# Optimization experiments

Hardware: AMD Instinct MI355X
Metric: run time of the kernel (lower is better)

## Reference

```python
import jax, jax.numpy as jnp
import numpy as np

N = 50000          # nodes
E = 800000         # edges per meta-path (avg degree 16)
M = 2              # meta-paths
IN = 256           # in_size
H, D = 4, 64       # heads, out_size per head
HD = H * D
SEM_HID = 128      # SemanticAttention hidden_size
NEG_SLOPE = 0.2    # DGL GATConv default LeakyReLU slope


def setup_inputs() -> dict:
    key = jax.random.key(0)
    ks = jax.random.split(key, 10)
    h = jax.random.normal(ks[0], (N, IN), dtype=jnp.float32)
    src = jax.random.randint(ks[1], (M, E), 0, N, dtype=jnp.int32)
    dst = jax.random.randint(ks[2], (M, E), 0, N, dtype=jnp.int32)
    # per-meta-path GATConv params
    W = jax.random.normal(ks[3], (M, IN, HD), dtype=jnp.float32) * (1.0 / np.sqrt(IN))
    attn_l = jax.random.normal(ks[4], (M, H, D), dtype=jnp.float32) * 0.1
    attn_r = jax.random.normal(ks[5], (M, H, D), dtype=jnp.float32) * 0.1
    # semantic attention params
    sem_w1 = jax.random.normal(ks[6], (HD, SEM_HID), dtype=jnp.float32) * (1.0 / np.sqrt(HD))
    sem_b1 = jnp.zeros((SEM_HID,), dtype=jnp.float32)
    sem_w2 = jax.random.normal(ks[7], (SEM_HID, 1), dtype=jnp.float32) * (1.0 / np.sqrt(SEM_HID))
    return {"h": h, "src": src, "dst": dst, "W": W, "attn_l": attn_l,
            "attn_r": attn_r, "sem_w1": sem_w1, "sem_b1": sem_b1, "sem_w2": sem_w2}


def _gat_conv(h, s, d, W_i, al, ar):
    # h: [N, IN]; s, d: [E] int edge endpoints; returns [N, H*D]
    feat = (h @ W_i).reshape(N, H, D)                       # [N,H,D]
    el = jnp.einsum('nhd,hd->nh', feat, al)                 # [N,H]
    er = jnp.einsum('nhd,hd->nh', feat, ar)                 # [N,H]
    e = jax.nn.leaky_relu(el[s] + er[d], NEG_SLOPE)         # [E,H]
    # edge softmax over incoming edges of each dst node
    m = jax.ops.segment_max(e, d, num_segments=N)           # [N,H]
    m = jax.lax.stop_gradient(jnp.where(jnp.isfinite(m), m, 0.0))
    ex = jnp.exp(e - m[d])                                  # [E,H]
    den = jax.ops.segment_sum(ex, d, num_segments=N)        # [N,H]
    alpha = ex / jnp.maximum(den[d], 1e-9)                  # [E,H]
    msg = alpha[:, :, None] * feat[s]                       # [E,H,D]
    rst = jax.ops.segment_sum(msg, d, num_segments=N)       # [N,H,D] (zero for 0-in-degree)
    return jax.nn.elu(rst).reshape(N, HD)


def reference(h, src, dst, W, attn_l, attn_r, sem_w1, sem_b1, sem_w2):
    embs = [_gat_conv(h, src[i], dst[i], W[i], attn_l[i], attn_r[i]) for i in range(M)]
    z = jnp.stack(embs, axis=1)                             # [N,M,HD]
    # semantic attention: w = mean over nodes of MLP score per meta-path
    w = jnp.einsum('nms,so->mo', jnp.tanh(jnp.einsum('nmd,ds->nms', z, sem_w1) + sem_b1), sem_w2) / N  # [M,1]
    beta = jax.nn.softmax(w, axis=0)                        # [M,1]
    return jnp.einsum('nmd,mo->nd', z, beta)                # [N,HD]
```

## Files before the change

kernel.cpp:

```cpp
#include <hip/hip_runtime.h>
#include <hip/hip_bf16.h>

#define NND 50000
#define NE 800000
#define NM 2
#define INF 256
#define NH 4
#define HDIM 256
#define SHID 128
#define SLOPE 0.2f
#define NB 196
#define NREP 8

typedef unsigned short u16;
typedef __attribute__((ext_vector_type(8))) short bf16x8;
typedef __attribute__((ext_vector_type(4))) float f32x4;

__device__ __forceinline__ float us2f(u16 u) {
  union { unsigned int i; float f; } v; v.i = ((unsigned int)u) << 16; return v.f;
}
__device__ __forceinline__ u16 f2us(float f) {
  union { float f; unsigned int i; } v; v.f = f;
  unsigned int r = v.i + 0x7FFFu + ((v.i >> 16) & 1u);
  return (u16)(r >> 16);
}

#define GLDS(g, l) __builtin_amdgcn_global_load_lds( \
    (const __attribute__((address_space(1))) unsigned int*)(g), \
    (__attribute__((address_space(3))) unsigned int*)(l), 16, 0, 0)

__global__ __launch_bounds__(256) void kh_cvt(const float* __restrict__ h,
                                              u16* __restrict__ hb) {
  const size_t i = ((size_t)blockIdx.x * 256 + threadIdx.x) * 8;
  float4 a = *(const float4*)(h + i);
  float4 b = *(const float4*)(h + i + 4);
  bf16x8 r;
  r[0] = f2us(a.x); r[1] = f2us(a.y); r[2] = f2us(a.z); r[3] = f2us(a.w);
  r[4] = f2us(b.x); r[5] = f2us(b.y); r[6] = f2us(b.z); r[7] = f2us(b.w);
  *(bf16x8*)(hb + i) = r;
}

__global__ __launch_bounds__(256) void kt_w(const float* __restrict__ W,
                                            u16* __restrict__ Wt) {
  __shared__ u16 tile[64][65];
  const int t = threadIdx.x;
  const int k0 = blockIdx.x * 64, n0 = blockIdx.y * 64;
  const float* Wm = W + (size_t)blockIdx.z * 65536;
  u16* Wtm = Wt + (size_t)blockIdx.z * 65536;
  const int lr = t >> 2, c0 = (t & 3) * 16;
#pragma unroll
  for (int i = 0; i < 16; ++i)
    tile[lr][c0 + i] = f2us(Wm[(size_t)(k0 + lr) * 256 + n0 + c0 + i]);
  __syncthreads();
#pragma unroll
  for (int i = 0; i < 16; ++i)
    Wtm[(size_t)(n0 + lr) * 256 + k0 + c0 + i] = tile[c0 + i][lr];
}

__global__ __launch_bounds__(256) void kt_w1(const float* __restrict__ w1,
                                             u16* __restrict__ w1t) {
  __shared__ u16 tile[64][65];
  const int t = threadIdx.x;
  const int k0 = blockIdx.x * 64, j0 = blockIdx.y * 64;
  const int lr = t >> 2, c0 = (t & 3) * 16;
#pragma unroll
  for (int i = 0; i < 16; ++i)
    tile[lr][c0 + i] = f2us(w1[(size_t)(k0 + lr) * SHID + j0 + c0 + i]);
  __syncthreads();
#pragma unroll
  for (int i = 0; i < 16; ++i)
    w1t[(size_t)(j0 + lr) * 256 + k0 + c0 + i] = tile[c0 + i][lr];
}

__global__ __launch_bounds__(256) void kc_hist_both(const int* __restrict__ dst_all,
                                                    int* __restrict__ hrep) {
  int e = blockIdx.x * 256 + threadIdx.x;
  int p = (e >= NE) ? 1 : 0;
  int rep = blockIdx.x & (NREP - 1);
  atomicAdd(hrep + ((size_t)p * NREP + rep) * (NND + 1) + dst_all[e] + 1, 1);
}

__global__ __launch_bounds__(256) void ks1(const int* __restrict__ hrep,
                                           int* __restrict__ rowptr,
                                           int* __restrict__ bsum) {
  __shared__ int wsums[4];
  const int t = threadIdx.x;
  const int p = blockIdx.x / NB, lb = blockIdx.x % NB;
  int* rp = rowptr + (size_t)p * (NND + 1);
  const int i = lb * 256 + t + 1;
  int v = 0;
  if (i <= NND) {
    const int* hp = hrep + (size_t)p * NREP * (NND + 1);
#pragma unroll
    for (int r = 0; r < NREP; ++r) v += hp[(size_t)r * (NND + 1) + i];
  }
  const int lane = t & 63, wid = t >> 6;
#pragma unroll
  for (int o = 1; o < 64; o <<= 1) {
    int u = __shfl_up(v, o, 64);
    if (lane >= o) v += u;
  }
  if (lane == 63) wsums[wid] = v;
  __syncthreads();
  if (t == 0) {
    int s = 0;
#pragma unroll
    for (int w = 0; w < 4; ++w) { int x = wsums[w]; wsums[w] = s; s += x; }
    bsum[blockIdx.x] = s;
  }
  __syncthreads();
  v += wsums[wid];
  if (i <= NND) rp[i] = v;
}

__global__ __launch_bounds__(256) void ks3(int* __restrict__ rowptr,
                                           const int* __restrict__ bsum,
                                           int* __restrict__ cursor) {
  __shared__ int redp[4];
  __shared__ int off_s;
  const int t = threadIdx.x;
  const int p = blockIdx.x / NB, lb = blockIdx.x % NB;
  int* rp = rowptr + (size_t)p * (NND + 1);
  int* cp = cursor + (size_t)p * NND;
  int partial = (t < lb) ? bsum[p * NB + t] : 0;
  const int lane = t & 63, wid = t >> 6;
#pragma unroll
  for (int o = 32; o; o >>= 1) partial += __shfl_xor(partial, o, 64);
  if (lane == 0) redp[wid] = partial;
  __syncthreads();
  if (t == 0) off_s = redp[0] + redp[1] + redp[2] + redp[3];
  __syncthreads();
  const int off = off_s;
  const int i = lb * 256 + t + 1;
  if (i <= NND) {
    int v = rp[i] + off;
    rp[i] = v;
    if (i < NND) cp[i] = v;
    if (i == 1) { cp[0] = 0; rp[0] = 0; }
  }
}

__global__ __launch_bounds__(256) void kc_scatter(
    const int* __restrict__ src, const int* __restrict__ dst,
    int* __restrict__ cursor, int* __restrict__ col,
    const float* __restrict__ el, const float* __restrict__ er,
    float* __restrict__ exps)
{
  int e = blockIdx.x * 256 + threadIdx.x;
  if (e >= NE) return;
  int s = src[e], d = dst[e];
  int pos = atomicAdd(cursor + d, 1);
  col[pos] = s;
  float4 a = *(const float4*)(el + s * 4);
  float4 b = *(const float4*)(er + d * 4);
  float4 r;
  float x;
  x = a.x + b.x; x = x > 0.f ? x : SLOPE * x; r.x = __expf(x);
  x = a.y + b.y; x = x > 0.f ? x : SLOPE * x; r.y = __expf(x);
  x = a.z + b.z; x = x > 0.f ? x : SLOPE * x; r.z = __expf(x);
  x = a.w + b.w; x = x > 0.f ? x : SLOPE * x; r.w = __expf(x);
  *(float4*)(exps + (size_t)pos * 4) = r;
}

__global__ __launch_bounds__(256) void k1_mfma(
    const u16* __restrict__ hb, const u16* __restrict__ Wt,
    u16* __restrict__ feat)
{
  __shared__ u16 As[128 * 32];
  __shared__ u16 Bs[128 * 32];
  const int t = threadIdx.x;
  const int lane = t & 63;
  const int w = t >> 6;
  const int wr = w >> 1, wc = w & 1;
  const int row0 = blockIdx.x * 128;
  const int col0 = blockIdx.y * 128;

  const int sr = t >> 2;
  const int skb = (t & 3) * 8;

  int ra0 = row0 + sr;       if (ra0 >= NND) ra0 = NND - 1;
  int ra1 = row0 + 64 + sr;  if (ra1 >= NND) ra1 = NND - 1;
  const int cb0 = col0 + sr, cb1 = col0 + 64 + sr;

  f32x4 acc[4][4];
#pragma unroll
  for (int i = 0; i < 4; ++i)
#pragma unroll
    for (int j = 0; j < 4; ++j) acc[i][j] = (f32x4){0.f, 0.f, 0.f, 0.f};

  for (int ks = 0; ks < 8; ++ks) {
    const int kb = ks * 32 + skb;
    __syncthreads();
    GLDS(hb + (size_t)ra0 * INF + kb, As + w * 512);
    GLDS(hb + (size_t)ra1 * INF + kb, As + 2048 + w * 512);
    GLDS(Wt + (size_t)cb0 * 256 + kb, Bs + w * 512);
    GLDS(Wt + (size_t)cb1 * 256 + kb, Bs + 2048 + w * 512);
    __syncthreads();
    bf16x8 af[4], bfr[4];
#pragma unroll
    for (int mi = 0; mi < 4; ++mi)
      af[mi] = *(const bf16x8*)(As + (wr * 64 + mi * 16 + (lane & 15)) * 32 + (lane >> 4) * 8);
#pragma unroll
    for (int ni = 0; ni < 4; ++ni)
      bfr[ni] = *(const bf16x8*)(Bs + (wc * 64 + ni * 16 + (lane & 15)) * 32 + (lane >> 4) * 8);
#pragma unroll
    for (int mi = 0; mi < 4; ++mi)
#pragma unroll
      for (int ni = 0; ni < 4; ++ni)
        acc[mi][ni] = __builtin_amdgcn_mfma_f32_16x16x32_bf16(af[mi], bfr[ni], acc[mi][ni], 0, 0, 0);
  }
#pragma unroll
  for (int mi = 0; mi < 4; ++mi) {
    const int r_base = row0 + wr * 64 + mi * 16 + (lane >> 4) * 4;
#pragma unroll
    for (int i = 0; i < 4; ++i) {
      const int r = r_base + i;
      if (r < NND) {
#pragma unroll
        for (int ni = 0; ni < 4; ++ni) {
          const int c = col0 + wc * 64 + ni * 16 + (lane & 15);
          feat[(size_t)r * HDIM + c] = f2us(acc[mi][ni][i]);
        }
      }
    }
  }
}

__global__ __launch_bounds__(256) void k1b_elr(
    const u16* __restrict__ feat,
    const float* __restrict__ al, const float* __restrict__ ar,
    float* __restrict__ el, float* __restrict__ er)
{
  const int n = blockIdx.x * 4 + (threadIdx.x >> 6);
  const int lane = threadIdx.x & 63;
  ushort4 f4 = *(const ushort4*)(feat + (size_t)n * HDIM + lane * 4);
  float4 a4 = *(const float4*)(al + lane * 4);
  float4 r4 = *(const float4*)(ar + lane * 4);
  float fl = us2f(f4.x) * a4.x + us2f(f4.y) * a4.y
           + us2f(f4.z) * a4.z + us2f(f4.w) * a4.w;
  float fr = us2f(f4.x) * r4.x + us2f(f4.y) * r4.y
           + us2f(f4.z) * r4.z + us2f(f4.w) * r4.w;
#pragma unroll
  for (int o = 1; o < 16; o <<= 1) {
    fl += __shfl_xor(fl, o, 64);
    fr += __shfl_xor(fr, o, 64);
  }
  if ((lane & 15) == 0) {
    el[n * 4 + (lane >> 4)] = fl;
    er[n * 4 + (lane >> 4)] = fr;
  }
}

template<int OBF>
__global__ __launch_bounds__(256) void k3_gather(
    const int* __restrict__ rowptr, const int* __restrict__ col,
    const float* __restrict__ exps,
    const u16* __restrict__ feat, void* __restrict__ z)
{
  const int d = blockIdx.x * 4 + (threadIdx.x >> 6);
  if (d >= NND) return;
  const int lane = threadIdx.x & 63;
  const int h = lane >> 4;
  const int sub = lane & 15;
  const int beg = rowptr[d], end = rowptr[d + 1];

  float den = 0.f;
  for (int j = beg + sub; j < end; j += 16)
    den += exps[(size_t)j * 4 + h];
#pragma unroll
  for (int o = 1; o < 16; o <<= 1) den += __shfl_xor(den, o, 64);
  const float inv = 1.f / fmaxf(den, 1e-9f);

  float a0 = 0.f, a1 = 0.f, a2 = 0.f, a3 = 0.f;
  int j = beg;
  for (; j + 3 < end; j += 4) {
    int s0 = col[j], s1 = col[j + 1], s2 = col[j + 2], s3 = col[j + 3];
    float p0 = exps[(size_t)j * 4 + h] * inv;
    float p1 = exps[(size_t)(j + 1) * 4 + h] * inv;
    float p2 = exps[(size_t)(j + 2) * 4 + h] * inv;
    float p3 = exps[(size_t)(j + 3) * 4 + h] * inv;
    const ushort4 f0 = *(const ushort4*)(feat + (size_t)s0 * HDIM + lane * 4);
    const ushort4 f1 = *(const ushort4*)(feat + (size_t)s1 * HDIM + lane * 4);
    const ushort4 f2 = *(const ushort4*)(feat + (size_t)s2 * HDIM + lane * 4);
    const ushort4 f3 = *(const ushort4*)(feat + (size_t)s3 * HDIM + lane * 4);
    a0 = fmaf(p0, us2f(f0.x), a0); a1 = fmaf(p0, us2f(f0.y), a1);
    a2 = fmaf(p0, us2f(f0.z), a2); a3 = fmaf(p0, us2f(f0.w), a3);
    a0 = fmaf(p1, us2f(f1.x), a0); a1 = fmaf(p1, us2f(f1.y), a1);
    a2 = fmaf(p1, us2f(f1.z), a2); a3 = fmaf(p1, us2f(f1.w), a3);
    a0 = fmaf(p2, us2f(f2.x), a0); a1 = fmaf(p2, us2f(f2.y), a1);
    a2 = fmaf(p2, us2f(f2.z), a2); a3 = fmaf(p2, us2f(f2.w), a3);
    a0 = fmaf(p3, us2f(f3.x), a0); a1 = fmaf(p3, us2f(f3.y), a1);
    a2 = fmaf(p3, us2f(f3.z), a2); a3 = fmaf(p3, us2f(f3.w), a3);
  }
  for (; j < end; ++j) {
    int s = col[j];
    float p = exps[(size_t)j * 4 + h] * inv;
    const ushort4 f4 = *(const ushort4*)(feat + (size_t)s * HDIM + lane * 4);
    a0 = fmaf(p, us2f(f4.x), a0); a1 = fmaf(p, us2f(f4.y), a1);
    a2 = fmaf(p, us2f(f4.z), a2); a3 = fmaf(p, us2f(f4.w), a3);
  }
  a0 = a0 > 0.f ? a0 : expf(a0) - 1.f;
  a1 = a1 > 0.f ? a1 : expf(a1) - 1.f;
  a2 = a2 > 0.f ? a2 : expf(a2) - 1.f;
  a3 = a3 > 0.f ? a3 : expf(a3) - 1.f;
  const size_t idx = (size_t)d * HDIM + lane * 4;
  if (OBF) {
    ushort4 r; r.x = f2us(a0); r.y = f2us(a1); r.z = f2us(a2); r.w = f2us(a3);
    *(ushort4*)((u16*)z + idx) = r;
  } else {
    float4 r; r.x = a0; r.y = a1; r.z = a2; r.w = a3;
    *(float4*)((float*)z + idx) = r;
  }
}

template<int ZBF>
__global__ __launch_bounds__(256) void k4_mfma(
    const void* __restrict__ zsrc, const u16* __restrict__ w1t,
    const float* __restrict__ b1, const float* __restrict__ w2,
    float* __restrict__ wsum, int midx)
{
  __shared__ u16 As[128 * 32];
  __shared__ u16 Bs[128 * 32];
  __shared__ float red[4];
  const int t = threadIdx.x;
  const int lane = t & 63;
  const int w = t >> 6;
  const int wr = w >> 1, wc = w & 1;
  const int row0 = blockIdx.x * 128;
  const int sr = t >> 2;
  const int skb = (t & 3) * 8;
  int ra0 = row0 + sr;       if (ra0 >= NND) ra0 = NND - 1;
  int ra1 = row0 + 64 + sr;  if (ra1 >= NND) ra1 = NND - 1;
  const int cb0 = sr, cb1 = 64 + sr;

  f32x4 acc[4][4];
#pragma unroll
  for (int i = 0; i < 4; ++i)
#pragma unroll
    for (int j = 0; j < 4; ++j) acc[i][j] = (f32x4){0.f, 0.f, 0.f, 0.f};

  for (int ks = 0; ks < 8; ++ks) {
    const int kb = ks * 32 + skb;
    __syncthreads();
    if (ZBF) {
      GLDS((const u16*)zsrc + (size_t)ra0 * HDIM + kb, As + w * 512);
      GLDS((const u16*)zsrc + (size_t)ra1 * HDIM + kb, As + 2048 + w * 512);
    } else {
      const float* zf = (const float*)zsrc;
      float4 a = *(const float4*)(zf + (size_t)ra0 * HDIM + kb);
      float4 b = *(const float4*)(zf + (size_t)ra0 * HDIM + kb + 4);
      bf16x8 r;
      r[0] = f2us(a.x); r[1] = f2us(a.y); r[2] = f2us(a.z); r[3] = f2us(a.w);
      r[4] = f2us(b.x); r[5] = f2us(b.y); r[6] = f2us(b.z); r[7] = f2us(b.w);
      *(bf16x8*)(As + sr * 32 + skb) = r;
      a = *(const float4*)(zf + (size_t)ra1 * HDIM + kb);
      b = *(const float4*)(zf + (size_t)ra1 * HDIM + kb + 4);
      r[0] = f2us(a.x); r[1] = f2us(a.y); r[2] = f2us(a.z); r[3] = f2us(a.w);
      r[4] = f2us(b.x); r[5] = f2us(b.y); r[6] = f2us(b.z); r[7] = f2us(b.w);
      *(bf16x8*)(As + (64 + sr) * 32 + skb) = r;
    }
    GLDS(w1t + (size_t)cb0 * 256 + kb, Bs + w * 512);
    GLDS(w1t + (size_t)cb1 * 256 + kb, Bs + 2048 + w * 512);
    __syncthreads();
    bf16x8 af[4], bfr[4];
#pragma unroll
    for (int mi = 0; mi < 4; ++mi)
      af[mi] = *(const bf16x8*)(As + (wr * 64 + mi * 16 + (lane & 15)) * 32 + (lane >> 4) * 8);
#pragma unroll
    for (int ni = 0; ni < 4; ++ni)
      bfr[ni] = *(const bf16x8*)(Bs + (wc * 64 + ni * 16 + (lane & 15)) * 32 + (lane >> 4) * 8);
#pragma unroll
    for (int mi = 0; mi < 4; ++mi)
#pragma unroll
      for (int ni = 0; ni < 4; ++ni)
        acc[mi][ni] = __builtin_amdgcn_mfma_f32_16x16x32_bf16(af[mi], bfr[ni], acc[mi][ni], 0, 0, 0);
  }
  float sum = 0.f;
#pragma unroll
  for (int ni = 0; ni < 4; ++ni) {
    const int c = wc * 64 + ni * 16 + (lane & 15);
    const float b1c = b1[c], w2c = w2[c];
#pragma unroll
    for (int mi = 0; mi < 4; ++mi) {
      const int r_base = row0 + wr * 64 + mi * 16 + (lane >> 4) * 4;
#pragma unroll
      for (int i = 0; i < 4; ++i) {
        if (r_base + i < NND)
          sum += tanhf(acc[mi][ni][i] + b1c) * w2c;
      }
    }
  }
#pragma unroll
  for (int o = 32; o; o >>= 1) sum += __shfl_xor(sum, o, 64);
  if (lane == 0) red[w] = sum;
  __syncthreads();
  if (t == 0) unsafeAtomicAdd(wsum + midx, red[0] + red[1] + red[2] + red[3]);
}

__global__ __launch_bounds__(256) void k5_out(
    float* __restrict__ out, const u16* __restrict__ z1,
    const float* __restrict__ wsum)
{
  const int i = blockIdx.x * 256 + threadIdx.x;
  float w0 = wsum[0] * (1.0f / NND);
  float w1v = wsum[1] * (1.0f / NND);
  float mx = fmaxf(w0, w1v);
  float e0 = expf(w0 - mx), e1 = expf(w1v - mx);
  float inv = 1.f / (e0 + e1);
  float b0 = e0 * inv, b1 = e1 * inv;
  float4 a = ((const float4*)out)[i];
  ushort4 zb = ((const ushort4*)z1)[i];
  float4 r;
  r.x = b0 * a.x + b1 * us2f(zb.x);
  r.y = b0 * a.y + b1 * us2f(zb.y);
  r.z = b0 * a.z + b1 * us2f(zb.z);
  r.w = b0 * a.w + b1 * us2f(zb.w);
  ((float4*)out)[i] = r;
}

extern "C" void kernel_launch(void* const* d_in, const int* in_sizes, int n_in,
                              void* d_out, int out_size, void* d_ws, size_t ws_size,
                              hipStream_t stream)
{
  const float* h  = (const float*)d_in[0];
  const int* src  = (const int*)d_in[1];
  const int* dst  = (const int*)d_in[2];
  const float* W  = (const float*)d_in[3];
  const float* al = (const float*)d_in[4];
  const float* ar = (const float*)d_in[5];
  const float* w1 = (const float*)d_in[6];
  const float* b1 = (const float*)d_in[7];
  const float* w2 = (const float*)d_in[8];

  char* wsb = (char*)d_ws;
  u16*   feat   = (u16*)(wsb);
  u16*   hz     = (u16*)(wsb + 25600000);
  float* exps   = (float*)(wsb + 51200000);
  int*   col    = (int*)(wsb + 64000000);
  u16*   Wt     = (u16*)(wsb + 67200000);
  u16*   w1t    = (u16*)(wsb + 67462144);
  float* el     = (float*)(wsb + 67527680);
  float* er     = (float*)(wsb + 68327680);
  int*   rowptr = (int*)(wsb + 69127680);
  int*   cursor = (int*)(wsb + 69527688);
  float* wsum   = (float*)(wsb + 69927688);
  int*   bsum   = (int*)(wsb + 69927696);
  int*   hrep   = (int*)(wsb + 69929264);
  const size_t NEED = 73129328;
  if (ws_size < NEED) {
    hipMemsetAsync(d_out, 0x7F, (size_t)out_size * 4, stream);
    return;
  }
  u16* z1 = hz;
  float* outp = (float*)d_out;

  kh_cvt<<<6250, 256, 0, stream>>>(h, hz);
  kt_w<<<dim3(4, 4, 2), 256, 0, stream>>>(W, Wt);
  kt_w1<<<dim3(4, 2), 256, 0, stream>>>(w1, w1t);
  hipMemsetAsync(wsum, 0, 2 * sizeof(float), stream);
  hipMemsetAsync(hrep, 0, (size_t)2 * NREP * (NND + 1) * sizeof(int), stream);
  kc_hist_both<<<2 * NE / 256, 256, 0, stream>>>(dst, hrep);
  ks1<<<2 * NB, 256, 0, stream>>>(hrep, rowptr, bsum);
  ks3<<<2 * NB, 256, 0, stream>>>(rowptr, bsum, cursor);

  for (int m = 0; m < NM; ++m) {
    const int* src_m = src + (size_t)m * NE;
    const int* dst_m = dst + (size_t)m * NE;
    int* rowptr_m = rowptr + (size_t)m * (NND + 1);
    int* cursor_m = cursor + (size_t)m * NND;
    k1_mfma<<<dim3(391, 2), 256, 0, stream>>>(hz, Wt + (size_t)m * 65536, feat);
    k1b_elr<<<12500, 256, 0, stream>>>(feat, al + (size_t)m * HDIM, ar + (size_t)m * HDIM, el, er);
    kc_scatter<<<NE / 256, 256, 0, stream>>>(src_m, dst_m, cursor_m, col, el, er, exps);
    if (m == 0) {
      k3_gather<0><<<12500, 256, 0, stream>>>(rowptr_m, col, exps, feat, d_out);
      k4_mfma<0><<<391, 256, 0, stream>>>(d_out, w1t, b1, w2, wsum, 0);
    } else {
      k3_gather<1><<<12500, 256, 0, stream>>>(rowptr_m, col, exps, feat, z1);
      k4_mfma<1><<<391, 256, 0, stream>>>(z1, w1t, b1, w2, wsum, 1);
    }
  }
  k5_out<<<(NND * HDIM / 4) / 256, 256, 0, stream>>>(outp, z1, wsum);
}
```

Before: 418.5 us.

## Merge prep kernels, split scatter cursors per replica, widen GEMM K-tiles with swizzle

Three setup kernels (input cast, W transpose, w1 transpose) are merged into one launch. The scatter step now uses NREP per-replica cursor arrays, seeded from the per-replica histograms, so fewer atomics contend on the same destination counter. Both MFMA GEMMs stage 64-wide K tiles with an XOR-swizzled LDS layout, which halves the number of K-loop iterations and barriers and avoids bank conflicts on fragment loads. This costs double the LDS per block and an extra cursor workspace.

Result: faster. 406.3 us (-2.9%).

```diff
diff --git a/kernel.cpp b/kernel.cpp
--- a/kernel.cpp
+++ b/kernel.cpp
@@ -29,47 +29,47 @@
     (const __attribute__((address_space(1))) unsigned int*)(g), \
     (__attribute__((address_space(3))) unsigned int*)(l), 16, 0, 0)
 
-__global__ __launch_bounds__(256) void kh_cvt(const float* __restrict__ h,
-                                              u16* __restrict__ hb) {
-  const size_t i = ((size_t)blockIdx.x * 256 + threadIdx.x) * 8;
-  float4 a = *(const float4*)(h + i);
-  float4 b = *(const float4*)(h + i + 4);
-  bf16x8 r;
-  r[0] = f2us(a.x); r[1] = f2us(a.y); r[2] = f2us(a.z); r[3] = f2us(a.w);
-  r[4] = f2us(b.x); r[5] = f2us(b.y); r[6] = f2us(b.z); r[7] = f2us(b.w);
-  *(bf16x8*)(hb + i) = r;
-}
-
-__global__ __launch_bounds__(256) void kt_w(const float* __restrict__ W,
-                                            u16* __restrict__ Wt) {
+__global__ __launch_bounds__(256) void kprep(
+    const float* __restrict__ h, u16* __restrict__ hb,
+    const float* __restrict__ W, u16* __restrict__ Wt,
+    const float* __restrict__ w1, u16* __restrict__ w1t)
+{
   __shared__ u16 tile[64][65];
   const int t = threadIdx.x;
-  const int k0 = blockIdx.x * 64, n0 = blockIdx.y * 64;
-  const float* Wm = W + (size_t)blockIdx.z * 65536;
-  u16* Wtm = Wt + (size_t)blockIdx.z * 65536;
-  const int lr = t >> 2, c0 = (t & 3) * 16;
-#pragma unroll
-  for (int i = 0; i < 16; ++i)
-    tile[lr][c0 + i] = f2us(Wm[(size_t)(k0 + lr) * 256 + n0 + c0 + i]);
-  __syncthreads();
-#pragma unroll
-  for (int i = 0; i < 16; ++i)
-    Wtm[(size_t)(n0 + lr) * 256 + k0 + c0 + i] = tile[c0 + i][lr];
-}
-
-__global__ __launch_bounds__(256) void kt_w1(const float* __restrict__ w1,
-                                             u16* __restrict__ w1t) {
-  __shared__ u16 tile[64][65];
-  const int t = threadIdx.x;
-  const int k0 = blockIdx.x * 64, j0 = blockIdx.y * 64;
-  const int lr = t >> 2, c0 = (t & 3) * 16;
-#pragma unroll
-  for (int i = 0; i < 16; ++i)
-    tile[lr][c0 + i] = f2us(w1[(size_t)(k0 + lr) * SHID + j0 + c0 + i]);
-  __syncthreads();
-#pragma unroll
-  for (int i = 0; i < 16; ++i)
-    w1t[(size_t)(j0 + lr) * 256 + k0 + c0 + i] = tile[c0 + i][lr];
+  const int bid = blockIdx.x;
+  if (bid < 6250) {
+    const size_t i = ((size_t)bid * 256 + t) * 8;
+    float4 a = *(const float4*)(h + i);
+    float4 b = *(const float4*)(h + i + 4);
+    bf16x8 r;
+    r[0] = f2us(a.x); r[1] = f2us(a.y); r[2] = f2us(a.z); r[3] = f2us(a.w);
+    r[4] = f2us(b.x); r[5] = f2us(b.y); r[6] = f2us(b.z); r[7] = f2us(b.w);
+    *(bf16x8*)(hb + i) = r;
+  } else if (bid < 6250 + 32) {
+    const int b = bid - 6250;
+    const int k0 = (b & 3) * 64, n0 = ((b >> 2) & 3) * 64;
+    const float* Wm = W + (size_t)(b >> 4) * 65536;
+    u16* Wtm = Wt + (size_t)(b >> 4) * 65536;
+    const int lr = t >> 2, c0 = (t & 3) * 16;
+#pragma unroll
+    for (int i = 0; i < 16; ++i)
+      tile[lr][c0 + i] = f2us(Wm[(size_t)(k0 + lr) * 256 + n0 + c0 + i]);
+    __syncthreads();
+#pragma unroll
+    for (int i = 0; i < 16; ++i)
+      Wtm[(size_t)(n0 + lr) * 256 + k0 + c0 + i] = tile[c0 + i][lr];
+  } else {
+    const int b = bid - 6282;
+    const int k0 = (b & 3) * 64, j0 = (b >> 2) * 64;
+    const int lr = t >> 2, c0 = (t & 3) * 16;
+#pragma unroll
+    for (int i = 0; i < 16; ++i)
+      tile[lr][c0 + i] = f2us(w1[(size_t)(k0 + lr) * SHID + j0 + c0 + i]);
+    __syncthreads();
+#pragma unroll
+    for (int i = 0; i < 16; ++i)
+      w1t[(size_t)(j0 + lr) * 256 + k0 + c0 + i] = tile[c0 + i][lr];
+  }
 }
 
 __global__ __launch_bounds__(256) void kc_hist_both(const int* __restrict__ dst_all,
@@ -115,13 +115,15 @@
 
 __global__ __launch_bounds__(256) void ks3(int* __restrict__ rowptr,
                                            const int* __restrict__ bsum,
-                                           int* __restrict__ cursor) {
+                                           const int* __restrict__ hrep,
+                                           int* __restrict__ crep) {
   __shared__ int redp[4];
   __shared__ int off_s;
   const int t = threadIdx.x;
   const int p = blockIdx.x / NB, lb = blockIdx.x % NB;
   int* rp = rowptr + (size_t)p * (NND + 1);
-  int* cp = cursor + (size_t)p * NND;
+  const int* hp = hrep + (size_t)p * NREP * (NND + 1);
+  int* cp = crep + (size_t)p * NREP * NND;
   int partial = (t < lb) ? bsum[p * NB + t] : 0;
   const int lane = t & 63, wid = t >> 6;
 #pragma unroll
@@ -135,21 +137,37 @@
   if (i <= NND) {
     int v = rp[i] + off;
     rp[i] = v;
-    if (i < NND) cp[i] = v;
-    if (i == 1) { cp[0] = 0; rp[0] = 0; }
+    if (i < NND) {
+      int cum = v;
+#pragma unroll
+      for (int r = 0; r < NREP; ++r) {
+        cp[(size_t)r * NND + i] = cum;
+        cum += hp[(size_t)r * (NND + 1) + i + 1];
+      }
+    }
+    if (i == 1) {
+      rp[0] = 0;
+      int cum = 0;
+#pragma unroll
+      for (int r = 0; r < NREP; ++r) {
+        cp[(size_t)r * NND + 0] = cum;
+        cum += hp[(size_t)r * (NND + 1) + 1];
+      }
+    }
   }
 }
 
 __global__ __launch_bounds__(256) void kc_scatter(
     const int* __restrict__ src, const int* __restrict__ dst,
-    int* __restrict__ cursor, int* __restrict__ col,
+    int* __restrict__ crep_m, int* __restrict__ col,
     const float* __restrict__ el, const float* __restrict__ er,
-    float* __restrict__ exps)
+    float* __restrict__ exps, int chunk0)
 {
   int e = blockIdx.x * 256 + threadIdx.x;
   if (e >= NE) return;
   int s = src[e], d = dst[e];
-  int pos = atomicAdd(cursor + d, 1);
+  int rep = (chunk0 + blockIdx.x) & (NREP - 1);
+  int pos = atomicAdd(crep_m + (size_t)rep * NND + d, 1);
   col[pos] = s;
   float4 a = *(const float4*)(el + s * 4);
   float4 b = *(const float4*)(er + d * 4);
@@ -166,8 +184,8 @@
     const u16* __restrict__ hb, const u16* __restrict__ Wt,
     u16* __restrict__ feat)
 {
-  __shared__ u16 As[128 * 32];
-  __shared__ u16 Bs[128 * 32];
+  __shared__ u16 As[128 * 64];
+  __shared__ u16 Bs[128 * 64];
   const int t = threadIdx.x;
   const int lane = t & 63;
   const int w = t >> 6;
@@ -175,12 +193,17 @@
   const int row0 = blockIdx.x * 128;
   const int col0 = blockIdx.y * 128;
 
-  const int sr = t >> 2;
-  const int skb = (t & 3) * 8;
-
-  int ra0 = row0 + sr;       if (ra0 >= NND) ra0 = NND - 1;
-  int ra1 = row0 + 64 + sr;  if (ra1 >= NND) ra1 = NND - 1;
-  const int cb0 = col0 + sr, cb1 = col0 + 64 + sr;
+  const int srow = t >> 3;
+  const int sg   = t & 7;
+  const int sgl  = (sg ^ (srow & 7)) * 8;
+
+  int ra[4], cb[4];
+#pragma unroll
+  for (int q = 0; q < 4; ++q) {
+    int r = row0 + q * 32 + srow; if (r >= NND) r = NND - 1;
+    ra[q] = r;
+    cb[q] = col0 + q * 32 + srow;
+  }
 
   f32x4 acc[4][4];
 #pragma unroll
@@ -188,26 +211,36 @@
 #pragma unroll
     for (int j = 0; j < 4; ++j) acc[i][j] = (f32x4){0.f, 0.f, 0.f, 0.f};
 
-  for (int ks = 0; ks < 8; ++ks) {
-    const int kb = ks * 32 + skb;
+  for (int ks = 0; ks < 4; ++ks) {
+    const int kb = ks * 64 + sgl;
     __syncthreads();
-    GLDS(hb + (size_t)ra0 * INF + kb, As + w * 512);
-    GLDS(hb + (size_t)ra1 * INF + kb, As + 2048 + w * 512);
-    GLDS(Wt + (size_t)cb0 * 256 + kb, Bs + w * 512);
-    GLDS(Wt + (size_t)cb1 * 256 + kb, Bs + 2048 + w * 512);
+#pragma unroll
+    for (int q = 0; q < 4; ++q) {
+      GLDS(hb + (size_t)ra[q] * INF + kb, As + q * 2048 + w * 512);
+      GLDS(Wt + (size_t)cb[q] * 256 + kb, Bs + q * 2048 + w * 512);
+    }
     __syncthreads();
-    bf16x8 af[4], bfr[4];
-#pragma unroll
-    for (int mi = 0; mi < 4; ++mi)
-      af[mi] = *(const bf16x8*)(As + (wr * 64 + mi * 16 + (lane & 15)) * 32 + (lane >> 4) * 8);
-#pragma unroll
-    for (int ni = 0; ni < 4; ++ni)
-      bfr[ni] = *(const bf16x8*)(Bs + (wc * 64 + ni * 16 + (lane & 15)) * 32 + (lane >> 4) * 8);
-#pragma unroll
-    for (int mi = 0; mi < 4; ++mi)
-#pragma unroll
-      for (int ni = 0; ni < 4; ++ni)
-        acc[mi][ni] = __builtin_amdgcn_mfma_f32_16x16x32_bf16(af[mi], bfr[ni], acc[mi][ni], 0, 0, 0);
+#pragma unroll
+    for (int kk = 0; kk < 2; ++kk) {
+      bf16x8 af[4], bfr[4];
+#pragma unroll
+      for (int mi = 0; mi < 4; ++mi) {
+        const int R = wr * 64 + mi * 16 + (lane & 15);
+        const int g = kk * 4 + (lane >> 4);
+        af[mi] = *(const bf16x8*)(As + R * 64 + (g ^ (R & 7)) * 8);
+      }
+#pragma unroll
+      for (int ni = 0; ni < 4; ++ni) {
+        const int R = wc * 64 + ni * 16 + (lane & 15);
+        const int g = kk * 4 + (lane >> 4);
+        bfr[ni] = *(const bf16x8*)(Bs + R * 64 + (g ^ (R & 7)) * 8);
+      }
+#pragma unroll
+      for (int mi = 0; mi < 4; ++mi)
+#pragma unroll
+        for (int ni = 0; ni < 4; ++ni)
+          acc[mi][ni] = __builtin_amdgcn_mfma_f32_16x16x32_bf16(af[mi], bfr[ni], acc[mi][ni], 0, 0, 0);
+    }
   }
 #pragma unroll
   for (int mi = 0; mi < 4; ++mi) {
@@ -319,19 +352,25 @@
     const float* __restrict__ b1, const float* __restrict__ w2,
     float* __restrict__ wsum, int midx)
 {
-  __shared__ u16 As[128 * 32];
-  __shared__ u16 Bs[128 * 32];
+  __shared__ u16 As[128 * 64];
+  __shared__ u16 Bs[128 * 64];
   __shared__ float red[4];
   const int t = threadIdx.x;
   const int lane = t & 63;
   const int w = t >> 6;
   const int wr = w >> 1, wc = w & 1;
   const int row0 = blockIdx.x * 128;
-  const int sr = t >> 2;
-  const int skb = (t & 3) * 8;
-  int ra0 = row0 + sr;       if (ra0 >= NND) ra0 = NND - 1;
-  int ra1 = row0 + 64 + sr;  if (ra1 >= NND) ra1 = NND - 1;
-  const int cb0 = sr, cb1 = 64 + sr;
+  const int srow = t >> 3;
+  const int sg   = t & 7;
+  const int sgl  = (sg ^ (srow & 7)) * 8;
+
+  int ra[4], cb[4];
+#pragma unroll
+  for (int q = 0; q < 4; ++q) {
+    int r = row0 + q * 32 + srow; if (r >= NND) r = NND - 1;
+    ra[q] = r;
+    cb[q] = q * 32 + srow;
+  }
 
   f32x4 acc[4][4];
 #pragma unroll
@@ -339,41 +378,50 @@
 #pragma unroll
     for (int j = 0; j < 4; ++j) acc[i][j] = (f32x4){0.f, 0.f, 0.f, 0.f};
 
-  for (int ks = 0; ks < 8; ++ks) {
-    const int kb = ks * 32 + skb;
+  for (int ks = 0; ks < 4; ++ks) {
+    const int kb = ks * 64 + sgl;
     __syncthreads();
     if (ZBF) {
-      GLDS((const u16*)zsrc + (size_t)ra0 * HDIM + kb, As + w * 512);
-      GLDS((const u16*)zsrc + (size_t)ra1 * HDIM + kb, As + 2048 + w * 512);
+#pragma unroll
+      for (int q = 0; q < 4; ++q)
+        GLDS((const u16*)zsrc + (size_t)ra[q] * HDIM + kb, As + q * 2048 + w * 512);
     } else {
       const float* zf = (const float*)zsrc;
-      float4 a = *(const float4*)(zf + (size_t)ra0 * HDIM + kb);
-      float4 b = *(const float4*)(zf + (size_t)ra0 * HDIM + kb + 4);
-      bf16x8 r;
-      r[0] = f2us(a.x); r[1] = f2us(a.y); r[2] = f2us(a.z); r[3] = f2us(a.w);
-      r[4] = f2us(b.x); r[5] = f2us(b.y); r[6] = f2us(b.z); r[7] = f2us(b.w);
-      *(bf16x8*)(As + sr * 32 + skb) = r;
-      a = *(const float4*)(zf + (size_t)ra1 * HDIM + kb);
-      b = *(const float4*)(zf + (size_t)ra1 * HDIM + kb + 4);
-      r[0] = f2us(a.x); r[1] = f2us(a.y); r[2] = f2us(a.z); r[3] = f2us(a.w);
-      r[4] = f2us(b.x); r[5] = f2us(b.y); r[6] = f2us(b.z); r[7] = f2us(b.w);
-      *(bf16x8*)(As + (64 + sr) * 32 + skb) = r;
-    }
-    GLDS(w1t + (size_t)cb0 * 256 + kb, Bs + w * 512);
-    GLDS(w1t + (size_t)cb1 * 256 + kb, Bs + 2048 + w * 512);
+#pragma unroll
+      for (int q = 0; q < 4; ++q) {
+        float4 a = *(const float4*)(zf + (size_t)ra[q] * HDIM + kb);
+        float4 b = *(const float4*)(zf + (size_t)ra[q] * HDIM + kb + 4);
+        bf16x8 r;
+        r[0] = f2us(a.x); r[1] = f2us(a.y); r[2] = f2us(a.z); r[3] = f2us(a.w);
+        r[4] = f2us(b.x); r[5] = f2us(b.y); r[6] = f2us(b.z); r[7] = f2us(b.w);
+        *(bf16x8*)(As + (q * 32 + srow) * 64 + (sg ^ (srow & 7)) * 8) = r;
+      }
+    }
+#pragma unroll
+    for (int q = 0; q < 4; ++q)
+      GLDS(w1t + (size_t)cb[q] * 256 + kb, Bs + q * 2048 + w * 512);
     __syncthreads();
-    bf16x8 af[4], bfr[4];
-#pragma unroll
-    for (int mi = 0; mi < 4; ++mi)
-      af[mi] = *(const bf16x8*)(As + (wr * 64 + mi * 16 + (lane & 15)) * 32 + (lane >> 4) * 8);
-#pragma unroll
-    for (int ni = 0; ni < 4; ++ni)
-      bfr[ni] = *(const bf16x8*)(Bs + (wc * 64 + ni * 16 + (lane & 15)) * 32 + (lane >> 4) * 8);
-#pragma unroll
-    for (int mi = 0; mi < 4; ++mi)
-#pragma unroll
-      for (int ni = 0; ni < 4; ++ni)
-        acc[mi][ni] = __builtin_amdgcn_mfma_f32_16x16x32_bf16(af[mi], bfr[ni], acc[mi][ni], 0, 0, 0);
+#pragma unroll
+    for (int kk = 0; kk < 2; ++kk) {
+      bf16x8 af[4], bfr[4];
+#pragma unroll
+      for (int mi = 0; mi < 4; ++mi) {
+        const int R = wr * 64 + mi * 16 + (lane & 15);
+        const int g = kk * 4 + (lane >> 4);
+        af[mi] = *(const bf16x8*)(As + R * 64 + (g ^ (R & 7)) * 8);
+      }
+#pragma unroll
+      for (int ni = 0; ni < 4; ++ni) {
+        const int R = wc * 64 + ni * 16 + (lane & 15);
+        const int g = kk * 4 + (lane >> 4);
+        bfr[ni] = *(const bf16x8*)(Bs + R * 64 + (g ^ (R & 7)) * 8);
+      }
+#pragma unroll
+      for (int mi = 0; mi < 4; ++mi)
+#pragma unroll
+        for (int ni = 0; ni < 4; ++ni)
+          acc[mi][ni] = __builtin_amdgcn_mfma_f32_16x16x32_bf16(af[mi], bfr[ni], acc[mi][ni], 0, 0, 0);
+    }
   }
   float sum = 0.f;
 #pragma unroll
@@ -442,11 +490,11 @@
   float* el     = (float*)(wsb + 67527680);
   float* er     = (float*)(wsb + 68327680);
   int*   rowptr = (int*)(wsb + 69127680);
-  int*   cursor = (int*)(wsb + 69527688);
-  float* wsum   = (float*)(wsb + 69927688);
-  int*   bsum   = (int*)(wsb + 69927696);
-  int*   hrep   = (int*)(wsb + 69929264);
-  const size_t NEED = 73129328;
+  float* wsum   = (float*)(wsb + 69527688);
+  int*   bsum   = (int*)(wsb + 69527696);
+  int*   hrep   = (int*)(wsb + 69529264);
+  int*   crep   = (int*)(wsb + 72729328);
+  const size_t NEED = 75929328;
   if (ws_size < NEED) {
     hipMemsetAsync(d_out, 0x7F, (size_t)out_size * 4, stream);
     return;
@@ -454,23 +502,21 @@
   u16* z1 = hz;
   float* outp = (float*)d_out;
 
-  kh_cvt<<<6250, 256, 0, stream>>>(h, hz);
-  kt_w<<<dim3(4, 4, 2), 256, 0, stream>>>(W, Wt);
-  kt_w1<<<dim3(4, 2), 256, 0, stream>>>(w1, w1t);
+  kprep<<<6290, 256, 0, stream>>>(h, hz, W, Wt, w1, w1t);
   hipMemsetAsync(wsum, 0, 2 * sizeof(float), stream);
   hipMemsetAsync(hrep, 0, (size_t)2 * NREP * (NND + 1) * sizeof(int), stream);
   kc_hist_both<<<2 * NE / 256, 256, 0, stream>>>(dst, hrep);
   ks1<<<2 * NB, 256, 0, stream>>>(hrep, rowptr, bsum);
-  ks3<<<2 * NB, 256, 0, stream>>>(rowptr, bsum, cursor);
+  ks3<<<2 * NB, 256, 0, stream>>>(rowptr, bsum, hrep, crep);
 
   for (int m = 0; m < NM; ++m) {
     const int* src_m = src + (size_t)m * NE;
     const int* dst_m = dst + (size_t)m * NE;
     int* rowptr_m = rowptr + (size_t)m * (NND + 1);
-    int* cursor_m = cursor + (size_t)m * NND;
+    int* crep_m   = crep + (size_t)m * NREP * NND;
     k1_mfma<<<dim3(391, 2), 256, 0, stream>>>(hz, Wt + (size_t)m * 65536, feat);
     k1b_elr<<<12500, 256, 0, stream>>>(feat, al + (size_t)m * HDIM, ar + (size_t)m * HDIM, el, er);
-    kc_scatter<<<NE / 256, 256, 0, stream>>>(src_m, dst_m, cursor_m, col, el, er, exps);
+    kc_scatter<<<NE / 256, 256, 0, stream>>>(src_m, dst_m, crep_m, col, el, er, exps, m * 3125);
     if (m == 0) {
       k3_gather<0><<<12500, 256, 0, stream>>>(rowptr_m, col, exps, feat, d_out);
       k4_mfma<0><<<391, 256, 0, stream>>>(d_out, w1t, b1, w2, wsum, 0);
```
